# Kernel optimization log

Hardware: AMD Instinct MI355X
Metric: run time of the kernel (lower is better)

Reference implementation:

```python
import jax, jax.numpy as jnp
import numpy as np

CHANNELS = 256
NUM_HEADS = 4
NUM_GROUPS = 8
EPS = 1e-5


def setup_inputs() -> dict:
    key = jax.random.key(0)
    ks = jax.random.split(key, 7)
    c = CHANNELS
    x = jax.random.normal(ks[0], (2, c, 16, 16, 16), dtype=jnp.float32)
    # GroupNorm affine params (torch init: weight=1, bias=0)
    norm_w = jnp.ones((c,), dtype=jnp.float32)
    norm_b = jnp.zeros((c,), dtype=jnp.float32)
    # 1x1x1 Conv3d weights stored as [out_ch, in_ch]
    fan = 1.0 / np.sqrt(c)
    qkv_w = jax.random.uniform(ks[1], (3 * c, c), minval=-fan, maxval=fan, dtype=jnp.float32)
    qkv_b = jax.random.uniform(ks[2], (3 * c,), minval=-fan, maxval=fan, dtype=jnp.float32)
    proj_w = jax.random.uniform(ks[3], (c, c), minval=-fan, maxval=fan, dtype=jnp.float32)
    proj_b = jax.random.uniform(ks[4], (c,), minval=-fan, maxval=fan, dtype=jnp.float32)
    return {"x": x, "norm_w": norm_w, "norm_b": norm_b,
            "qkv_w": qkv_w, "qkv_b": qkv_b, "proj_w": proj_w, "proj_b": proj_b}


def _group_norm(x, w, b):
    B, C, D, H, W = x.shape
    g = NUM_GROUPS
    xg = x.reshape(B, g, C // g, D, H, W)
    mean = xg.mean(axis=(2, 3, 4, 5), keepdims=True)
    var = xg.var(axis=(2, 3, 4, 5), keepdims=True)
    xg = (xg - mean) * jax.lax.rsqrt(var + EPS)
    x = xg.reshape(B, C, D, H, W)
    return x * w[None, :, None, None, None] + b[None, :, None, None, None]


def _conv1x1(x, w, b):
    # x: [B, Cin, D, H, W], w: [Cout, Cin]
    y = jnp.einsum('bcdhw,oc->bodhw', x, w)
    return y + b[None, :, None, None, None]


def reference(x, norm_w, norm_b, qkv_w, qkv_b, proj_w, proj_b):
    B, C, D, H, W = x.shape
    N = D * H * W
    hd = C // NUM_HEADS
    x_norm = _group_norm(x, norm_w, norm_b)
    qkv = _conv1x1(x_norm, qkv_w, qkv_b)  # [B, 3C, D, H, W]
    q, k, v = jnp.split(qkv, 3, axis=1)
    q = q.reshape(B, NUM_HEADS, hd, N)
    k = k.reshape(B, NUM_HEADS, hd, N)
    v = v.reshape(B, NUM_HEADS, hd, N)
    scale = hd ** -0.5
    # attn[b,h,n,m] = softmax_m(q[:, :, :, n] . k[:, :, :, m] * scale)
    scores = jnp.einsum('bhcn,bhcm->bhnm', q, k) * scale
    attn = jax.nn.softmax(scores, axis=-1)
    out = jnp.einsum('bhcm,bhnm->bhcn', v, attn)
    out = out.reshape(B, C, D, H, W)
    return _conv1x1(out, proj_w, proj_b) + x
```

## Files before the change

### kernel.cpp

```cpp
#include <hip/hip_runtime.h>
#include <hip/hip_bf16.h>

#define NSP 4096
#define CH 256
#define NB 2
#define NG 8
#define CPG 32
#define NHD 4
#define HDIM 64

typedef unsigned short u16;
typedef unsigned int u32;
typedef __attribute__((ext_vector_type(8))) short bf16x8;
typedef __attribute__((ext_vector_type(4))) float f32x4;
typedef __attribute__((ext_vector_type(16))) float f32x16;
typedef __attribute__((ext_vector_type(2))) unsigned int u32x2;
typedef __attribute__((ext_vector_type(4))) unsigned int u32x4;

#define MFMA __builtin_amdgcn_mfma_f32_16x16x32_bf16
#define MFMA32 __builtin_amdgcn_mfma_f32_32x32x16_bf16
#define QSCALE 0.18033688f

__device__ __forceinline__ u16 f2bf(float f) {
    u32 i = __float_as_uint(f);
    u32 r = (i + 0x7FFFu + ((i >> 16) & 1u)) >> 16;
    return (u16)r;
}

__device__ __forceinline__ void dma16(const u16* g, u16* l) {
    __builtin_amdgcn_global_load_lds(
        (const __attribute__((address_space(1))) void*)g,
        (__attribute__((address_space(3))) void*)l, 16, 0, 0);
}

__device__ __forceinline__ void plswap(u32& a, u32& b) {
#if __has_builtin(__builtin_amdgcn_permlane32_swap)
    u32x2 r = __builtin_amdgcn_permlane32_swap(a, b, false, false);
    a = r.x; b = r.y;
#else
    u32 sa = (u32)__shfl_xor((int)a, 32);
    u32 sb = (u32)__shfl_xor((int)b, 32);
    bool hi = (threadIdx.x & 32) != 0;
    u32 na = hi ? sb : a;
    u32 nb = hi ? b : sa;
    a = na; b = nb;
#endif
}

__global__ __launch_bounds__(256) void prep(const float* __restrict__ qw,
                                            const float* __restrict__ pw,
                                            u16* __restrict__ wqb,
                                            u16* __restrict__ wpb,
                                            const float* __restrict__ x,
                                            float* __restrict__ partial) {
    if (blockIdx.x < 256) {
        int i = (blockIdx.x * 256 + threadIdx.x) * 4;
        const float* src; u16* dstbase; int j;
        if (i < 3 * CH * CH) { src = qw + i; dstbase = wqb; j = i; }
        else { j = i - 3 * CH * CH; src = pw + j; dstbase = wpb; }
        int m = j >> 8, c = j & 255;
        int dc = ((((c >> 3) ^ (m & 7)) << 3)) | (c & 7);
        float4 v = *(const float4*)src;
        ushort4 o;
        o.x = f2bf(v.x); o.y = f2bf(v.y); o.z = f2bf(v.z); o.w = f2bf(v.w);
        *(ushort4*)(dstbase + (m << 8) + dc) = o;
        return;
    }
    const int id = blockIdx.x - 256;
    const int bg = id >> 4, chunk = id & 15;
    const float* p = x + (size_t)bg * (CPG * NSP) + chunk * 8192;
    float s = 0.f, ss = 0.f;
    for (int i = threadIdx.x; i < 2048; i += 256) {
        float4 u = ((const float4*)p)[i];
        s += u.x + u.y + u.z + u.w;
        ss += u.x * u.x + u.y * u.y + u.z * u.z + u.w * u.w;
    }
    for (int off = 32; off > 0; off >>= 1) {
        s += __shfl_down(s, off);
        ss += __shfl_down(ss, off);
    }
    __shared__ float red[4][2];
    const int wv = threadIdx.x >> 6;
    if ((threadIdx.x & 63) == 0) { red[wv][0] = s; red[wv][1] = ss; }
    __syncthreads();
    if (threadIdx.x == 0) {
        float ts = red[0][0] + red[1][0] + red[2][0] + red[3][0];
        float tq = red[0][1] + red[1][1] + red[2][1] + red[3][1];
        partial[(bg * 16 + chunk) * 2]     = ts;
        partial[(bg * 16 + chunk) * 2 + 1] = tq;
    }
}

__global__ __launch_bounds__(256) void gn_apply_t(const float* __restrict__ x,
                                                  const float* __restrict__ partial,
                                                  const float* __restrict__ w,
                                                  const float* __restrict__ b,
                                                  u16* __restrict__ xnT) {
    __shared__ u16 T[64][72];
    const int n0 = blockIdx.x * 64, c0 = blockIdx.y * 64, bb = blockIdx.z;
    const int t = threadIdx.x;
    const int rc = t & 63;
    const int g  = t >> 6;
    const int c  = c0 + rc;
    const int bg = bb * NG + c / CPG;
    float s = 0.f, q = 0.f;
#pragma unroll
    for (int j = 0; j < 16; ++j) {
        s += partial[(bg * 16 + j) * 2];
        q += partial[(bg * 16 + j) * 2 + 1];
    }
    const float cnt = (float)(CPG * NSP);
    float mean = s / cnt;
    float var  = q / cnt - mean * mean;
    float rstd = rsqrtf(var + 1e-5f);
    float wf = w[c] * rstd, bv = b[c] - mean * wf;
    const float* px = x + ((size_t)bb * CH + c) * NSP + n0 + g * 16;
#pragma unroll
    for (int i = 0; i < 4; ++i) {
        float4 v = *(const float4*)(px + i * 4);
        T[g * 16 + i * 4 + 0][rc] = f2bf(v.x * wf + bv);
        T[g * 16 + i * 4 + 1][rc] = f2bf(v.y * wf + bv);
        T[g * 16 + i * 4 + 2][rc] = f2bf(v.z * wf + bv);
        T[g * 16 + i * 4 + 3][rc] = f2bf(v.w * wf + bv);
    }
    __syncthreads();
    int n = t >> 2, ch = (t & 3) * 16;
    uint4 o0 = *(const uint4*)&T[n][ch];
    uint4 o1 = *(const uint4*)&T[n][ch + 8];
    const int sw = n & 7;
    const int chunk0 = (c0 + ch) >> 3;
    u16* rowp = xnT + ((size_t)bb * NSP + n0 + n) * CH;
    *(uint4*)(rowp + ((chunk0 ^ sw) << 3))       = o0;
    *(uint4*)(rowp + (((chunk0 + 1) ^ sw) << 3)) = o1;
}

__global__ __launch_bounds__(256, 2) void gemm_qkv(const u16* __restrict__ Aw,
                                                   const float* __restrict__ bias,
                                                   const u16* __restrict__ xnT,
                                                   u16* __restrict__ qT,
                                                   u16* __restrict__ kT,
                                                   u16* __restrict__ v) {
    __shared__ u16 As[64][256];
    __shared__ u16 Bs[64][256];
    const int n0 = blockIdx.x * 64, m0 = blockIdx.y * 64, bb = blockIdx.z;
    const int wave = threadIdx.x >> 6, lane = threadIdx.x & 63;
    const int lq = lane & 15, quad = lane >> 4;
#pragma unroll
    for (int j = 0; j < 8; ++j) {
        int r2 = (wave * 8 + j) * 2;
        dma16(Aw + (size_t)(m0 + r2) * CH + lane * 8, &As[r2][0]);
        dma16(xnT + ((size_t)bb * NSP + n0 + r2) * CH + lane * 8, &Bs[r2][0]);
    }
    __syncthreads();
    const int wm = (wave >> 1) * 32, wn = (wave & 1) * 32;
    const int sw = lq & 7;
    f32x4 acc[2][2] = {};
#pragma unroll
    for (int kk = 0; kk < 8; ++kk) {
        bf16x8 a[2], b[2];
#pragma unroll
        for (int mt = 0; mt < 2; ++mt)
            a[mt] = *(const bf16x8*)&As[wm + mt * 16 + lq][(((kk * 4 + quad) ^ sw)) << 3];
#pragma unroll
        for (int nt = 0; nt < 2; ++nt)
            b[nt] = *(const bf16x8*)&Bs[wn + nt * 16 + lq][(((kk * 4 + quad) ^ sw)) << 3];
#pragma unroll
        for (int mt = 0; mt < 2; ++mt)
#pragma unroll
            for (int nt = 0; nt < 2; ++nt)
                acc[mt][nt] = MFMA(a[mt], b[nt], acc[mt][nt], 0, 0, 0);
    }
    const int sect = m0 >> 8;
    const int h = (m0 & 255) >> 6;
    const float osc = (sect == 0) ? QSCALE : 1.f;
#pragma unroll
    for (int im = 0; im < 2; ++im) {
        int ml = wm + im * 16 + quad * 4;
        float4 bs = *(const float4*)(bias + m0 + ml);
#pragma unroll
        for (int in = 0; in < 2; ++in) {
            int n = n0 + wn + in * 16 + lq;
            f32x4 a = acc[im][in];
            float v0 = (a[0] + bs.x) * osc, v1 = (a[1] + bs.y) * osc;
            float v2 = (a[2] + bs.z) * osc, v3 = (a[3] + bs.w) * osc;
            if (sect < 2) {
                int lc = ml >> 3, sub = ml & 7;
                int colp = ((lc ^ (n & 7)) << 3) | sub;
                u16* base = (sect ? kT : qT) +
                            (((size_t)bb * NHD + h) * NSP + n) * HDIM + colp;
                ushort4 o;
                o.x = f2bf(v0); o.y = f2bf(v1); o.z = f2bf(v2); o.w = f2bf(v3);
                *(ushort4*)base = o;
            } else {
                float vv[4] = {v0, v1, v2, v3};
#pragma unroll
                for (int r = 0; r < 4; ++r) {
                    int ch = (m0 - 512) + ml + r;
                    int pos = (n & ~63) + ((((n >> 3) & 7) ^ (ch & 7)) << 3) + (n & 7);
                    v[((size_t)bb * CH + ch) * NSP + pos] = f2bf(vv[r]);
                }
            }
        }
    }
}

__global__ __launch_bounds__(512, 2) void attn12(const u16* __restrict__ qT,
                                                 const u16* __restrict__ kT,
                                                 const u16* __restrict__ vN,
                                                 u16* __restrict__ aoT) {
    __shared__ __align__(16) char smem[131072];
    u16 (*Ks)[2][64][64] = reinterpret_cast<u16(*)[2][64][64]>(smem);
    u16 (*Vs)[2][64][64] = reinterpret_cast<u16(*)[2][64][64]>(smem + 65536);

    const int h = blockIdx.y, bb = blockIdx.z;
    const int t = threadIdx.x;
    const int wave = t >> 6, lane = t & 63;
    const int l31 = lane & 31, hi = lane >> 5, ln7 = lane & 7;
    const int qg = wave >> 2;
    const int csl = wave & 3;
    const int q_lo = blockIdx.x * 128 + qg * 64;

    bf16x8 qf[2][4];
#pragma unroll
    for (int qt = 0; qt < 2; ++qt) {
        const u16* qrow = qT + (((size_t)bb * NHD + h) * NSP + q_lo + qt * 32 + l31) * HDIM;
#pragma unroll
        for (int d = 0; d < 4; ++d)
            qf[qt][d] = *(const bf16x8*)(qrow + (((d * 2 + hi) ^ ln7) << 3));
    }

    const u16* khead = kT + ((size_t)bb * NHD + h) * NSP * (size_t)HDIM;
    const u16* vhead = vN + ((size_t)bb * CH + h * HDIM) * NSP;

    const int sV  = wave >> 2;
    const int ssl = wave & 3;
    int koff[4];
#pragma unroll
    for (int d = 0; d < 4; ++d) koff[d] = (((d * 2 + hi) ^ ln7) << 3);

#pragma unroll
    for (int j = 0; j < 8; ++j) {
        if (sV == 0)
            dma16(khead + (size_t)(ssl * 1024 + j * 8) * HDIM + lane * 8,
                  &Ks[ssl][0][j * 8][0]);
        else
            dma16(vhead + (size_t)(j * 8 + (lane >> 3)) * NSP + ssl * 1024 + (lane & 7) * 8,
                  &Vs[ssl][0][j * 8][0]);
    }

    float l[2] = {0.f, 0.f};
    f32x16 O[2][2] = {};
    for (int kt = 0; kt < 16; ++kt) {
        const int cur = kt & 1;
        __syncthreads();
        if (kt < 15) {
            const int K1 = (kt + 1) * 64;
#pragma unroll
            for (int j = 0; j < 8; ++j) {
                if (sV == 0)
                    dma16(khead + (size_t)(ssl * 1024 + K1 + j * 8) * HDIM + lane * 8,
                          &Ks[ssl][cur ^ 1][j * 8][0]);
                else
                    dma16(vhead + (size_t)(j * 8 + (lane >> 3)) * NSP + ssl * 1024 + K1 + (lane & 7) * 8,
                          &Vs[ssl][cur ^ 1][j * 8][0]);
            }
        }
#pragma unroll
        for (int ktile = 0; ktile < 2; ++ktile) {
            u32x4 pf[2][2];
#pragma unroll
            for (int qt = 0; qt < 2; ++qt) {
                f32x16 acc = {};
#pragma unroll
                for (int d = 0; d < 4; ++d) {
                    bf16x8 kf = *(const bf16x8*)&Ks[csl][cur][ktile * 32 + l31][koff[d]];
                    acc = MFMA32(kf, qf[qt][d], acc, 0, 0, 0);
                }
                float sum = 0.f;
                u32 pk_[8];
#pragma unroll
                for (int g = 0; g < 4; ++g) {
                    float p0 = __builtin_amdgcn_exp2f(acc[4 * g + 0]);
                    float p1 = __builtin_amdgcn_exp2f(acc[4 * g + 1]);
                    float p2 = __builtin_amdgcn_exp2f(acc[4 * g + 2]);
                    float p3 = __builtin_amdgcn_exp2f(acc[4 * g + 3]);
                    sum += (p0 + p1) + (p2 + p3);
                    u32 r0 = __float_as_uint(p0) + 0x8000u;
                    u32 r1 = __float_as_uint(p1) + 0x8000u;
                    u32 r2 = __float_as_uint(p2) + 0x8000u;
                    u32 r3 = __float_as_uint(p3) + 0x8000u;
                    pk_[2 * g]     = __builtin_amdgcn_perm(r1, r0, 0x07060302);
                    pk_[2 * g + 1] = __builtin_amdgcn_perm(r3, r2, 0x07060302);
                }
                l[qt] += sum;
                plswap(pk_[0], pk_[2]); plswap(pk_[1], pk_[3]);
                plswap(pk_[4], pk_[6]); plswap(pk_[5], pk_[7]);
                pf[qt][0][0] = pk_[0]; pf[qt][0][1] = pk_[1];
                pf[qt][0][2] = pk_[2]; pf[qt][0][3] = pk_[3];
                pf[qt][1][0] = pk_[4]; pf[qt][1][1] = pk_[5];
                pf[qt][1][2] = pk_[6]; pf[qt][1][3] = pk_[7];
            }
#pragma unroll
            for (int ct = 0; ct < 2; ++ct)
#pragma unroll
                for (int s = 0; s < 2; ++s) {
                    bf16x8 vf = *(const bf16x8*)
                        &Vs[csl][cur][ct * 32 + l31][(((ktile * 4 + s * 2 + hi) ^ ln7) << 3)];
                    bf16x8 pb0 = __builtin_bit_cast(bf16x8, pf[0][s]);
                    bf16x8 pb1 = __builtin_bit_cast(bf16x8, pf[1][s]);
                    O[0][ct] = MFMA32(vf, pb0, O[0][ct], 0, 0, 0);
                    O[1][ct] = MFMA32(vf, pb1, O[1][ct], 0, 0, 0);
                }
        }
    }
    l[0] += __shfl_xor(l[0], 32);
    l[1] += __shfl_xor(l[1], 32);
    __syncthreads();
    float* ob  = (float*)smem;
    float* MlA = (float*)(smem + 65536);
    if (lane < 32) {
        MlA[(wave * 2 + 0) * 32 + l31] = l[0];
        MlA[(wave * 2 + 1) * 32 + l31] = l[1];
    }
    if (csl >= 2) {
        int slot = qg * 2 + (csl - 2);
#pragma unroll
        for (int qt = 0; qt < 2; ++qt)
#pragma unroll
            for (int ct = 0; ct < 2; ++ct) {
                float* sp = ob + slot * 4096 + ((qt * 2 + ct) * 64 + lane) * 16;
#pragma unroll
                for (int cc = 0; cc < 4; ++cc) {
                    f32x4 tmp = {O[qt][ct][4 * cc + 0], O[qt][ct][4 * cc + 1],
                                 O[qt][ct][4 * cc + 2], O[qt][ct][4 * cc + 3]};
                    *(f32x4*)(sp + ((cc ^ (lane & 3)) << 2)) = tmp;
                }
            }
    }
    __syncthreads();
    if (csl < 2) {
        int slot = qg * 2 + csl;
#pragma unroll
        for (int qt = 0; qt < 2; ++qt)
#pragma unroll
            for (int ct = 0; ct < 2; ++ct) {
                float* sp = ob + slot * 4096 + ((qt * 2 + ct) * 64 + lane) * 16;
#pragma unroll
                for (int cc = 0; cc < 4; ++cc) {
                    f32x4 tmp = *(const f32x4*)(sp + ((cc ^ (lane & 3)) << 2));
                    O[qt][ct][4 * cc + 0] += tmp[0]; O[qt][ct][4 * cc + 1] += tmp[1];
                    O[qt][ct][4 * cc + 2] += tmp[2]; O[qt][ct][4 * cc + 3] += tmp[3];
                }
            }
    }
    __syncthreads();
    if (csl == 1) {
#pragma unroll
        for (int qt = 0; qt < 2; ++qt)
#pragma unroll
            for (int ct = 0; ct < 2; ++ct) {
                float* sp = ob + qg * 4096 + ((qt * 2 + ct) * 64 + lane) * 16;
#pragma unroll
                for (int cc = 0; cc < 4; ++cc) {
                    f32x4 tmp = {O[qt][ct][4 * cc + 0], O[qt][ct][4 * cc + 1],
                                 O[qt][ct][4 * cc + 2], O[qt][ct][4 * cc + 3]};
                    *(f32x4*)(sp + ((cc ^ (lane & 3)) << 2)) = tmp;
                }
            }
    }
    __syncthreads();
    if (csl == 0) {
#pragma unroll
        for (int qt = 0; qt < 2; ++qt)
#pragma unroll
            for (int ct = 0; ct < 2; ++ct) {
                float* sp = ob + qg * 4096 + ((qt * 2 + ct) * 64 + lane) * 16;
#pragma unroll
                for (int cc = 0; cc < 4; ++cc) {
                    f32x4 tmp = *(const f32x4*)(sp + ((cc ^ (lane & 3)) << 2));
                    O[qt][ct][4 * cc + 0] += tmp[0]; O[qt][ct][4 * cc + 1] += tmp[1];
                    O[qt][ct][4 * cc + 2] += tmp[2]; O[qt][ct][4 * cc + 3] += tmp[3];
                }
            }
        float gl[2], linv[2];
#pragma unroll
        for (int qt = 0; qt < 2; ++qt) {
            gl[qt] = l[qt]
                   + MlA[((qg * 4 + 1) * 2 + qt) * 32 + l31]
                   + MlA[((qg * 4 + 2) * 2 + qt) * 32 + l31]
                   + MlA[((qg * 4 + 3) * 2 + qt) * 32 + l31];
            linv[qt] = 1.f / gl[qt];
        }
#pragma unroll
        for (int qt = 0; qt < 2; ++qt) {
            u16* rowp = aoT + ((size_t)bb * NSP + q_lo + qt * 32 + l31) * CH;
#pragma unroll
            for (int ct = 0; ct < 2; ++ct)
#pragma unroll
                for (int g = 0; g < 4; ++g) {
                    ushort4 o;
                    o.x = f2bf(O[qt][ct][4 * g + 0] * linv[qt]);
                    o.y = f2bf(O[qt][ct][4 * g + 1] * linv[qt]);
                    o.z = f2bf(O[qt][ct][4 * g + 2] * linv[qt]);
                    o.w = f2bf(O[qt][ct][4 * g + 3] * linv[qt]);
                    int chunk = h * 8 + ct * 4 + g;
                    *(ushort4*)(rowp + ((chunk ^ ln7) << 3) + (hi << 2)) = o;
                }
        }
    }
}

__global__ __launch_bounds__(256, 2) void gemm_proj(const u16* __restrict__ Aw,
                                                    const float* __restrict__ bias,
                                                    const u16* __restrict__ aoT,
                                                    const float* __restrict__ xres,
                                                    float* __restrict__ out) {
    __shared__ u16 As[64][256];
    __shared__ u16 Bs[64][256];
    const int n0 = blockIdx.x * 64, m0 = blockIdx.y * 64, bb = blockIdx.z;
    const int wave = threadIdx.x >> 6, lane = threadIdx.x & 63;
    const int lq = lane & 15, quad = lane >> 4;
#pragma unroll
    for (int j = 0; j < 8; ++j) {
        int r2 = (wave * 8 + j) * 2;
        dma16(Aw + (size_t)(m0 + r2) * CH + lane * 8, &As[r2][0]);
        dma16(aoT + ((size_t)bb * NSP + n0 + r2) * CH + lane * 8, &Bs[r2][0]);
    }
    __syncthreads();
    const int wm = (wave >> 1) * 32, wn = (wave & 1) * 32;
    const int sw = lq & 7;
    f32x4 acc[2][2] = {};
#pragma unroll
    for (int kk = 0; kk < 8; ++kk) {
        bf16x8 a[2], b[2];
#pragma unroll
        for (int mt = 0; mt < 2; ++mt)
            a[mt] = *(const bf16x8*)&As[wm + mt * 16 + lq][(((kk * 4 + quad) ^ sw)) << 3];
#pragma unroll
        for (int nt = 0; nt < 2; ++nt)
            b[nt] = *(const bf16x8*)&Bs[wn + nt * 16 + lq][(((kk * 4 + quad) ^ sw)) << 3];
#pragma unroll
        for (int mt = 0; mt < 2; ++mt)
#pragma unroll
            for (int nt = 0; nt < 2; ++nt)
                acc[mt][nt] = MFMA(a[mt], b[nt], acc[mt][nt], 0, 0, 0);
    }
#pragma unroll
    for (int im = 0; im < 2; ++im) {
        int ml = wm + im * 16 + quad * 4;
        float4 bs = *(const float4*)(bias + m0 + ml);
        float bsv[4] = {bs.x, bs.y, bs.z, bs.w};
#pragma unroll
        for (int in = 0; in < 2; ++in) {
            int n = n0 + wn + in * 16 + lq;
            f32x4 a = acc[im][in];
#pragma unroll
            for (int r = 0; r < 4; ++r) {
                size_t idx = ((size_t)bb * CH + m0 + ml + r) * NSP + n;
                out[idx] = a[r] + bsv[r] + xres[idx];
            }
        }
    }
}

extern "C" void kernel_launch(void* const* d_in, const int* in_sizes, int n_in,
                              void* d_out, int out_size, void* d_ws, size_t ws_size,
                              hipStream_t stream) {
    const float* x      = (const float*)d_in[0];
    const float* norm_w = (const float*)d_in[1];
    const float* norm_b = (const float*)d_in[2];
    const float* qkv_w  = (const float*)d_in[3];
    const float* qkv_b  = (const float*)d_in[4];
    const float* proj_w = (const float*)d_in[5];
    const float* proj_b = (const float*)d_in[6];
    float* out = (float*)d_out;

    char* w = (char*)d_ws;
    float* partial = (float*)w;
    u16* wqb = (u16*)(w + 4096);
    u16* wpb = (u16*)(w + 4096 + 393216);
    u16* xnT = (u16*)(w + 528384);
    u16* qT  = (u16*)(w + 528384 + 4194304);
    u16* kT  = (u16*)(w + 528384 + 2 * 4194304);
    u16* v   = (u16*)(w + 528384 + 3 * 4194304);
    u16* aoT = xnT;

    prep<<<dim3(512), 256, 0, stream>>>(qkv_w, proj_w, wqb, wpb, x, partial);
    gn_apply_t<<<dim3(NSP / 64, CH / 64, NB), 256, 0, stream>>>(
        x, partial, norm_w, norm_b, xnT);
    gemm_qkv<<<dim3(NSP / 64, (3 * CH) / 64, NB), 256, 0, stream>>>(
        wqb, qkv_b, xnT, qT, kT, v);
    attn12<<<dim3(NSP / 128, NHD, NB), 512, 0, stream>>>(qT, kT, v, aoT);
    gemm_proj<<<dim3(NSP / 64, CH / 64, NB), 256, 0, stream>>>(
        wpb, proj_b, aoT, x, out);
}
```

Before: 133.0 us.

## Remap attention blocks per XCD, hoist LDS fragment loads, prioritize MFMA waves

The attention kernel now derives head and batch from the linear block id modulo 8, so every block for a given (batch, head) pair is scheduled on the same XCD and shares K/V in that die's L2. K and V fragments are loaded from LDS into registers before their MFMA chains, and s_setprio raises wave priority while those chains issue. The partial-output reduction through shared memory switches from an XOR-swizzled layout to a plain lane-strided layout. In exchange, register pressure rises, and the new reduction layout could change how LDS bank conflicts behave.

```diff
diff --git a/kernel.cpp b/kernel.cpp
--- a/kernel.cpp
+++ b/kernel.cpp
@@ -204,7 +204,7 @@
     }
 }
 
-__global__ __launch_bounds__(512, 2) void attn12(const u16* __restrict__ qT,
+__global__ __launch_bounds__(512, 2) void attn13(const u16* __restrict__ qT,
                                                  const u16* __restrict__ kT,
                                                  const u16* __restrict__ vN,
                                                  u16* __restrict__ aoT) {
@@ -212,13 +212,16 @@
     u16 (*Ks)[2][64][64] = reinterpret_cast<u16(*)[2][64][64]>(smem);
     u16 (*Vs)[2][64][64] = reinterpret_cast<u16(*)[2][64][64]>(smem + 65536);
 
-    const int h = blockIdx.y, bb = blockIdx.z;
+    const int id  = blockIdx.x + 32 * (blockIdx.y + 4 * blockIdx.z);
+    const int xcd = id & 7, loc = id >> 3;
+    const int h = xcd & 3, bb = xcd >> 2;
+
     const int t = threadIdx.x;
     const int wave = t >> 6, lane = t & 63;
     const int l31 = lane & 31, hi = lane >> 5, ln7 = lane & 7;
     const int qg = wave >> 2;
     const int csl = wave & 3;
-    const int q_lo = blockIdx.x * 128 + qg * 64;
+    const int q_lo = loc * 128 + qg * 64;
 
     bf16x8 qf[2][4];
 #pragma unroll
@@ -267,15 +270,19 @@
         }
 #pragma unroll
         for (int ktile = 0; ktile < 2; ++ktile) {
+            bf16x8 kf[4];
+#pragma unroll
+            for (int d = 0; d < 4; ++d)
+                kf[d] = *(const bf16x8*)&Ks[csl][cur][ktile * 32 + l31][koff[d]];
             u32x4 pf[2][2];
 #pragma unroll
             for (int qt = 0; qt < 2; ++qt) {
                 f32x16 acc = {};
-#pragma unroll
-                for (int d = 0; d < 4; ++d) {
-                    bf16x8 kf = *(const bf16x8*)&Ks[csl][cur][ktile * 32 + l31][koff[d]];
-                    acc = MFMA32(kf, qf[qt][d], acc, 0, 0, 0);
-                }
+                __builtin_amdgcn_s_setprio(1);
+#pragma unroll
+                for (int d = 0; d < 4; ++d)
+                    acc = MFMA32(kf[d], qf[qt][d], acc, 0, 0, 0);
+                __builtin_amdgcn_s_setprio(0);
                 float sum = 0.f;
                 u32 pk_[8];
 #pragma unroll
@@ -300,17 +307,24 @@
                 pf[qt][1][0] = pk_[4]; pf[qt][1][1] = pk_[5];
                 pf[qt][1][2] = pk_[6]; pf[qt][1][3] = pk_[7];
             }
+            bf16x8 vf[2][2];
+#pragma unroll
+            for (int ct = 0; ct < 2; ++ct)
+#pragma unroll
+                for (int s = 0; s < 2; ++s)
+                    vf[ct][s] = *(const bf16x8*)
+                        &Vs[csl][cur][ct * 32 + l31][(((ktile * 4 + s * 2 + hi) ^ ln7) << 3)];
+            __builtin_amdgcn_s_setprio(1);
 #pragma unroll
             for (int ct = 0; ct < 2; ++ct)
 #pragma unroll
                 for (int s = 0; s < 2; ++s) {
-                    bf16x8 vf = *(const bf16x8*)
-                        &Vs[csl][cur][ct * 32 + l31][(((ktile * 4 + s * 2 + hi) ^ ln7) << 3)];
                     bf16x8 pb0 = __builtin_bit_cast(bf16x8, pf[0][s]);
                     bf16x8 pb1 = __builtin_bit_cast(bf16x8, pf[1][s]);
-                    O[0][ct] = MFMA32(vf, pb0, O[0][ct], 0, 0, 0);
-                    O[1][ct] = MFMA32(vf, pb1, O[1][ct], 0, 0, 0);
-                }
+                    O[0][ct] = MFMA32(vf[ct][s], pb0, O[0][ct], 0, 0, 0);
+                    O[1][ct] = MFMA32(vf[ct][s], pb1, O[1][ct], 0, 0, 0);
+                }
+            __builtin_amdgcn_s_setprio(0);
         }
     }
     l[0] += __shfl_xor(l[0], 32);
@@ -323,65 +337,59 @@
         MlA[(wave * 2 + 1) * 32 + l31] = l[1];
     }
     if (csl >= 2) {
-        int slot = qg * 2 + (csl - 2);
+        float* sp = ob + (qg * 2 + (csl - 2)) * 4096;
 #pragma unroll
         for (int qt = 0; qt < 2; ++qt)
 #pragma unroll
-            for (int ct = 0; ct < 2; ++ct) {
-                float* sp = ob + slot * 4096 + ((qt * 2 + ct) * 64 + lane) * 16;
+            for (int ct = 0; ct < 2; ++ct)
 #pragma unroll
                 for (int cc = 0; cc < 4; ++cc) {
                     f32x4 tmp = {O[qt][ct][4 * cc + 0], O[qt][ct][4 * cc + 1],
                                  O[qt][ct][4 * cc + 2], O[qt][ct][4 * cc + 3]};
-                    *(f32x4*)(sp + ((cc ^ (lane & 3)) << 2)) = tmp;
-                }
-            }
+                    *(f32x4*)(sp + (((qt * 2 + ct) * 4 + cc) * 64 + lane) * 4) = tmp;
+                }
     }
     __syncthreads();
     if (csl < 2) {
-        int slot = qg * 2 + csl;
+        float* sp = ob + (qg * 2 + csl) * 4096;
 #pragma unroll
         for (int qt = 0; qt < 2; ++qt)
 #pragma unroll
-            for (int ct = 0; ct < 2; ++ct) {
-                float* sp = ob + slot * 4096 + ((qt * 2 + ct) * 64 + lane) * 16;
+            for (int ct = 0; ct < 2; ++ct)
 #pragma unroll
                 for (int cc = 0; cc < 4; ++cc) {
-                    f32x4 tmp = *(const f32x4*)(sp + ((cc ^ (lane & 3)) << 2));
+                    f32x4 tmp = *(const f32x4*)(sp + (((qt * 2 + ct) * 4 + cc) * 64 + lane) * 4);
                     O[qt][ct][4 * cc + 0] += tmp[0]; O[qt][ct][4 * cc + 1] += tmp[1];
                     O[qt][ct][4 * cc + 2] += tmp[2]; O[qt][ct][4 * cc + 3] += tmp[3];
                 }
-            }
     }
     __syncthreads();
     if (csl == 1) {
+        float* sp = ob + qg * 4096;
 #pragma unroll
         for (int qt = 0; qt < 2; ++qt)
 #pragma unroll
-            for (int ct = 0; ct < 2; ++ct) {
-                float* sp = ob + qg * 4096 + ((qt * 2 + ct) * 64 + lane) * 16;
+            for (int ct = 0; ct < 2; ++ct)
 #pragma unroll
                 for (int cc = 0; cc < 4; ++cc) {
                     f32x4 tmp = {O[qt][ct][4 * cc + 0], O[qt][ct][4 * cc + 1],
                                  O[qt][ct][4 * cc + 2], O[qt][ct][4 * cc + 3]};
-                    *(f32x4*)(sp + ((cc ^ (lane & 3)) << 2)) = tmp;
-                }
-            }
+                    *(f32x4*)(sp + (((qt * 2 + ct) * 4 + cc) * 64 + lane) * 4) = tmp;
+                }
     }
     __syncthreads();
     if (csl == 0) {
+        float* sp = ob + qg * 4096;
 #pragma unroll
         for (int qt = 0; qt < 2; ++qt)
 #pragma unroll
-            for (int ct = 0; ct < 2; ++ct) {
-                float* sp = ob + qg * 4096 + ((qt * 2 + ct) * 64 + lane) * 16;
+            for (int ct = 0; ct < 2; ++ct)
 #pragma unroll
                 for (int cc = 0; cc < 4; ++cc) {
-                    f32x4 tmp = *(const f32x4*)(sp + ((cc ^ (lane & 3)) << 2));
+                    f32x4 tmp = *(const f32x4*)(sp + (((qt * 2 + ct) * 4 + cc) * 64 + lane) * 4);
                     O[qt][ct][4 * cc + 0] += tmp[0]; O[qt][ct][4 * cc + 1] += tmp[1];
                     O[qt][ct][4 * cc + 2] += tmp[2]; O[qt][ct][4 * cc + 3] += tmp[3];
                 }
-            }
         float gl[2], linv[2];
 #pragma unroll
         for (int qt = 0; qt < 2; ++qt) {
@@ -490,7 +498,7 @@
         x, partial, norm_w, norm_b, xnT);
     gemm_qkv<<<dim3(NSP / 64, (3 * CH) / 64, NB), 256, 0, stream>>>(
         wqb, qkv_b, xnT, qT, kT, v);
-    attn12<<<dim3(NSP / 128, NHD, NB), 512, 0, stream>>>(qT, kT, v, aoT);
+    attn13<<<dim3(NSP / 128, NHD, NB), 512, 0, stream>>>(qT, kT, v, aoT);
     gemm_proj<<<dim3(NSP / 64, CH / 64, NB), 256, 0, stream>>>(
         wpb, proj_b, aoT, x, out);
 }
```

After: 136.1 us. 2.3% more time.
